# Kernel optimization log

Measured on AMD Instinct MI355X. Metric: run time of the kernel, lower is better.

Reference implementation:

```python
import jax, jax.numpy as jnp
import numpy as np

B = 512
IN_CORES = 12      # input_eff_capsules = 3072/256
N_PRIM = 12        # num_primary_capsules
N_PAR = 10         # num_parent_capsules
RFPC = 4           # receptive fields per capsule = 256/64
RF = 64            # receptive field size
CAP = 256          # capsule size
P_CONN = 0.2


def setup_inputs() -> dict:
    key = jax.random.key(0)
    ks = jax.random.split(key, 16)
    x = jax.random.uniform(ks[0], (B, 32, 32, 3), dtype=jnp.float32)
    # sparse 0/1 routing tensors (fixed Bernoulli(p) connectivity, stored as float params)
    C1 = jax.random.bernoulli(ks[1], P_CONN, (IN_CORES, RFPC, N_PRIM, RFPC)).astype(jnp.float32)
    C_skip = jax.random.bernoulli(ks[2], P_CONN, (IN_CORES, RFPC, N_PAR, RFPC)).astype(jnp.float32)
    C2 = jax.random.bernoulli(ks[3], P_CONN, (N_PRIM, RFPC, N_PAR, RFPC)).astype(jnp.float32)
    # per-receptive-field linear weights of the capsule layers
    s = 1.0 / np.sqrt(RF)
    W1 = jax.random.normal(ks[4], (N_PRIM, RFPC, RF, RF), dtype=jnp.float32) * s
    b1 = jnp.zeros((N_PRIM, RFPC, RF), dtype=jnp.float32)
    W2 = jax.random.normal(ks[5], (N_PAR, RFPC, RF, RF), dtype=jnp.float32) * s
    b2 = jnp.zeros((N_PAR, RFPC, RF), dtype=jnp.float32)
    # reconstruction MLP: 2560 -> 5000 -> 4000 -> 3072
    Wr1 = jax.random.normal(ks[6], (2560, 5000), dtype=jnp.float32) * (1.0 / np.sqrt(2560))
    br1 = jnp.zeros((5000,), dtype=jnp.float32)
    Wr2 = jax.random.normal(ks[7], (5000, 4000), dtype=jnp.float32) * (1.0 / np.sqrt(5000))
    br2 = jnp.zeros((4000,), dtype=jnp.float32)
    Wr3 = jax.random.normal(ks[8], (4000, 3072), dtype=jnp.float32) * (1.0 / np.sqrt(4000))
    br3 = jnp.zeros((3072,), dtype=jnp.float32)
    return {"x": x, "C1": C1, "W1": W1, "b1": b1, "C_skip": C_skip,
            "C2": C2, "W2": W2, "b2": b2,
            "Wr1": Wr1, "br1": br1, "Wr2": Wr2, "br2": br2, "Wr3": Wr3, "br3": br3}


def _caps_layer(x_flat, C, W, b):
    # x_flat: (B, in_cores*RFPC*RF); C: (in_cores, RFPC, out_caps, RFPC)
    bsz = x_flat.shape[0]
    in_cores = C.shape[0]
    xr = x_flat.reshape(bsz, in_cores, RFPC, RF)
    routed = jnp.einsum('ijkl,bijm->bklm', C, xr)          # (B, out_caps, RFPC, RF)
    out = jax.nn.relu(jnp.einsum('bklm,klmn->bkln', routed, W) + b)
    return out.reshape(bsz, -1)


def reference(x, C1, W1, b1, C_skip, C2, W2, b2, Wr1, br1, Wr2, br2, Wr3, br3):
    bsz = x.shape[0]
    # spatial_block_reshape: pure reshapes -> flatten
    x_flat = x.reshape(bsz, -1)                             # (B, 3072)
    # primary capsule layer
    x_prim = _caps_layer(x_flat, C1, W1, b1)                # (B, 3072)
    # skip connection: sparse routing einsum input->parent
    xr = x_prim.reshape(bsz, IN_CORES, RFPC, RF)
    x_skip = jnp.einsum('ijkl,bijm->bklm', C_skip, xr).reshape(bsz, -1)  # (B, 2560)
    # parent capsule layer + skip
    x_sum = x_skip + _caps_layer(x_prim, C2, W2, b2)        # (B, 2560)
    # top-1 capsule mask by norm
    norms = jnp.linalg.norm(x_sum.reshape(bsz, N_PAR, CAP), axis=-1)  # (B, 10)
    active = jnp.argmax(norms, axis=-1)                     # (B,)
    cap_id = jnp.arange(N_PAR * CAP) // CAP                 # (2560,)
    mask = (cap_id[None, :] == active[:, None]).astype(x_sum.dtype)
    x_recon = mask * x_sum
    # reconstruction MLP
    h = jax.nn.relu(x_recon @ Wr1 + br1)
    h = jax.nn.relu(h @ Wr2 + br2)
    out = jax.nn.sigmoid(h @ Wr3 + br3)                     # (B, 3072)
    return (out, x_sum)
```

## Files before the change

### kernel.cpp

```cpp
#include <hip/hip_runtime.h>
#include <math.h>


#define BATCH 512
#define OUT0_SZ (512*3072)

typedef __attribute__((ext_vector_type(8))) short short8;
typedef __attribute__((ext_vector_type(4))) float f32x4;

__device__ inline unsigned short f2bf(float f) {
    union { float f; unsigned u; } v; v.f = f;
    unsigned r = v.u + 0x7fffu + ((v.u >> 16) & 1u);
    return (unsigned short)(r >> 16);
}
__device__ inline float bf2f(unsigned int hi16) {
    union { unsigned u; float f; } v; v.u = hi16 << 16; return v.f;
}

#define GLD16(g, l) __builtin_amdgcn_global_load_lds( \
    (const __attribute__((address_space(1))) unsigned int*)(g), \
    (__attribute__((address_space(3))) unsigned int*)(l), 16, 0, 0)

struct CTJob {
    const float* W; unsigned short* Wt;
    int Kr, Nr, Kp, k0, n0;
};

__device__ inline CTJob ct_resolve(int bid,
    const float* Wr1, unsigned short* Wt1,
    const float* Wr2, unsigned short* Wt2,
    const float* Wr3, unsigned short* Wt3,
    const float* W1,  unsigned short* W1t,
    const float* W2,  unsigned short* W2t)
{
    CTJob j;
    int ktiles, rem;
    if (bid < 3200)       { j.W = Wr1; j.Wt = Wt1; j.Kr = 2560; j.Nr = 5000; j.Kp = 2560; ktiles = 40; rem = bid; }
    else if (bid < 8320)  { j.W = Wr2; j.Wt = Wt2; j.Kr = 5000; j.Nr = 4000; j.Kp = 5120; ktiles = 80; rem = bid - 3200; }
    else if (bid < 11392) { j.W = Wr3; j.Wt = Wt3; j.Kr = 4000; j.Nr = 3072; j.Kp = 4096; ktiles = 64; rem = bid - 8320; }
    else if (bid < 11440) { int kl = bid - 11392; j.W = W1 + (size_t)kl * 4096; j.Wt = W1t + (size_t)kl * 4096;
                            j.Kr = 64; j.Nr = 64; j.Kp = 64; ktiles = 1; rem = 0; }
    else                  { int kl = bid - 11440; j.W = W2 + (size_t)kl * 4096; j.Wt = W2t + (size_t)kl * 4096;
                            j.Kr = 64; j.Nr = 64; j.Kp = 64; ktiles = 1; rem = 0; }
    j.k0 = (rem % ktiles) * 64;
    j.n0 = (rem / ktiles) * 64;
    return j;
}

__device__ inline void ct_load(const CTJob& j, int tid, float4* v) {
    int kr = tid >> 4;
    int nc = (tid & 15) * 4;
    #pragma unroll
    for (int p = 0; p < 4; ++p) {
        int k = j.k0 + kr + p * 16;
        float4 vv = make_float4(0.f, 0.f, 0.f, 0.f);
        if (k < j.Kr) {
            if (j.n0 + nc + 3 < j.Nr) {
                vv = *(const float4*)&j.W[(size_t)k * j.Nr + j.n0 + nc];
            } else {
                float tmp[4] = {0.f, 0.f, 0.f, 0.f};
                #pragma unroll
                for (int jj = 0; jj < 4; ++jj)
                    if (j.n0 + nc + jj < j.Nr) tmp[jj] = j.W[(size_t)k * j.Nr + j.n0 + nc + jj];
                vv = make_float4(tmp[0], tmp[1], tmp[2], tmp[3]);
            }
        }
        v[p] = vv;
    }
}

__device__ inline void ct_stlds(float* t, int tid, const float4* v) {
    int kr = tid >> 4;
    int nc = (tid & 15) * 4;
    #pragma unroll
    for (int p = 0; p < 4; ++p) {
        float* row = &t[(kr + p * 16) * 65 + nc];
        row[0] = v[p].x; row[1] = v[p].y; row[2] = v[p].z; row[3] = v[p].w;
    }
}

__device__ inline void ct_pack(const CTJob& j, const float* t, int tid) {
    int nr = tid >> 2;
    int kc = (tid & 3) * 16;
    unsigned int u[8];
    #pragma unroll
    for (int jj = 0; jj < 8; ++jj) {
        float v0 = t[(kc + 2 * jj)     * 65 + nr];
        float v1 = t[(kc + 2 * jj + 1) * 65 + nr];
        u[jj] = (unsigned int)f2bf(v0) | ((unsigned int)f2bf(v1) << 16);
    }
    unsigned int* dst = (unsigned int*)&j.Wt[(size_t)(j.n0 + nr) * j.Kp + j.k0 + kc];
    *(uint4*)(dst)     = make_uint4(u[0], u[1], u[2], u[3]);
    *(uint4*)(dst + 4) = make_uint4(u[4], u[5], u[6], u[7]);
}

__global__ __launch_bounds__(256) void convT_all(
    const float* __restrict__ Wr1, unsigned short* __restrict__ Wt1,
    const float* __restrict__ Wr2, unsigned short* __restrict__ Wt2,
    const float* __restrict__ Wr3, unsigned short* __restrict__ Wt3,
    const float* __restrict__ W1,  unsigned short* __restrict__ W1t,
    const float* __restrict__ W2,  unsigned short* __restrict__ W2t)
{
    __shared__ float t[2][64 * 65];
    int tid = threadIdx.x;
    int tbase = blockIdx.x * 4;

    CTJob jc = ct_resolve(tbase, Wr1, Wt1, Wr2, Wt2, Wr3, Wt3, W1, W1t, W2, W2t);
    float4 v[4];
    ct_load(jc, tid, v);
    ct_stlds(t[0], tid, v);
    __syncthreads();

    #pragma unroll
    for (int i = 0; i < 4; ++i) {
        CTJob jn;
        float4 vn[4];
        if (i < 3) {
            jn = ct_resolve(tbase + i + 1, Wr1, Wt1, Wr2, Wt2, Wr3, Wt3, W1, W1t, W2, W2t);
            ct_load(jn, tid, vn);
        }
        ct_pack(jc, t[i & 1], tid);
        if (i < 3) {
            ct_stlds(t[(i + 1) & 1], tid, vn);
            jc = jn;
        }
        __syncthreads();
    }
}

__global__ __launch_bounds__(256) void caps_gemm1(
    const float* __restrict__ x, const float* __restrict__ C1,
    const unsigned short* __restrict__ W1t, const float* __restrict__ b1,
    unsigned short* __restrict__ xp)
{
    __shared__ __align__(16) unsigned short As[128 * 72];
    __shared__ __align__(16) unsigned short Bs[64 * 72];
    __shared__ float Csh[48];
    int kl = blockIdx.x;
    int bm = blockIdx.y * 128;
    int tid = threadIdx.x;
    int w = tid >> 6, lane = tid & 63, q = lane >> 4, r16 = lane & 15;
    int wm = (w >> 1) * 64, wn = (w & 1) * 32;

    if (tid < 48) Csh[tid] = C1[tid * 48 + kl];
    {
        const uint4* src = (const uint4*)(W1t + (size_t)kl * 4096);
        #pragma unroll
        for (int p = 0; p < 2; ++p) {
            int c = tid + p * 256;
            int row = c >> 3, cq = c & 7;
            *(uint4*)&Bs[row * 72 + cq * 8] = src[c];
        }
    }
    __syncthreads();

    int arow = tid >> 1, ah = (tid & 1) * 32;
    float accp[32];
    #pragma unroll
    for (int i = 0; i < 32; ++i) accp[i] = 0.f;
    const float* xrow = x + (size_t)(bm + arow) * 3072 + ah;
    for (int ij = 0; ij < 48; ++ij) {
        float c = Csh[ij];
        if (c != 0.f) {
            const float4* p4 = (const float4*)(xrow + ij * 64);
            #pragma unroll
            for (int cc = 0; cc < 8; ++cc) {
                float4 v = p4[cc];
                accp[cc * 4 + 0] = fmaf(c, v.x, accp[cc * 4 + 0]);
                accp[cc * 4 + 1] = fmaf(c, v.y, accp[cc * 4 + 1]);
                accp[cc * 4 + 2] = fmaf(c, v.z, accp[cc * 4 + 2]);
                accp[cc * 4 + 3] = fmaf(c, v.w, accp[cc * 4 + 3]);
            }
        }
    }
    {
        unsigned short* dst = &As[arow * 72 + ah];
        #pragma unroll
        for (int cc = 0; cc < 4; ++cc) {
            unsigned int u[4];
            #pragma unroll
            for (int j = 0; j < 4; ++j)
                u[j] = (unsigned int)f2bf(accp[cc * 8 + 2 * j]) |
                       ((unsigned int)f2bf(accp[cc * 8 + 2 * j + 1]) << 16);
            *(uint4*)&dst[cc * 8] = make_uint4(u[0], u[1], u[2], u[3]);
        }
    }
    __syncthreads();

    f32x4 acc[4][2];
    #pragma unroll
    for (int i = 0; i < 4; ++i)
        #pragma unroll
        for (int j = 0; j < 2; ++j) acc[i][j] = (f32x4)0.f;
    #pragma unroll
    for (int ks = 0; ks < 2; ++ks) {
        short8 a[4], b[2];
        #pragma unroll
        for (int mt = 0; mt < 4; ++mt)
            a[mt] = *(const short8*)&As[(wm + mt * 16 + r16) * 72 + ks * 32 + q * 8];
        #pragma unroll
        for (int nt = 0; nt < 2; ++nt)
            b[nt] = *(const short8*)&Bs[(wn + nt * 16 + r16) * 72 + ks * 32 + q * 8];
        #pragma unroll
        for (int mt = 0; mt < 4; ++mt)
            #pragma unroll
            for (int nt = 0; nt < 2; ++nt)
                acc[mt][nt] = __builtin_amdgcn_mfma_f32_16x16x32_bf16(a[mt], b[nt], acc[mt][nt], 0, 0, 0);
    }

    #pragma unroll
    for (int mt = 0; mt < 4; ++mt) {
        #pragma unroll
        for (int nt = 0; nt < 2; ++nt) {
            int n = wn + nt * 16 + r16;
            float bv = b1[kl * 64 + n];
            #pragma unroll
            for (int reg = 0; reg < 4; ++reg) {
                int row = bm + wm + mt * 16 + q * 4 + reg;
                xp[(size_t)row * 3072 + kl * 64 + n] = f2bf(fmaxf(acc[mt][nt][reg] + bv, 0.f));
            }
        }
    }
}

__global__ __launch_bounds__(256) void caps_gemm2(
    const unsigned short* __restrict__ xp, const float* __restrict__ Cs,
    const float* __restrict__ C2, const unsigned short* __restrict__ W2t,
    const float* __restrict__ b2, float* __restrict__ xsum,
    float* __restrict__ part8)
{
    __shared__ __align__(16) unsigned short As[128 * 72];
    __shared__ __align__(16) unsigned short Bs[64 * 72];
    __shared__ __align__(16) float Sk[128 * 68];
    __shared__ float C2sh[48], Cssh[48];
    int kl = blockIdx.x;
    int bm = blockIdx.y * 128;
    int tid = threadIdx.x;
    int w = tid >> 6, lane = tid & 63, q = lane >> 4, r16 = lane & 15;
    int wm = (w >> 1) * 64, wn = (w & 1) * 32;
    int half = w & 1;

    if (tid < 48) { C2sh[tid] = C2[tid * 40 + kl]; Cssh[tid] = Cs[tid * 40 + kl]; }
    {
        const uint4* src = (const uint4*)(W2t + (size_t)kl * 4096);
        #pragma unroll
        for (int p = 0; p < 2; ++p) {
            int c = tid + p * 256;
            int row = c >> 3, cq = c & 7;
            *(uint4*)&Bs[row * 72 + cq * 8] = src[c];
        }
    }
    __syncthreads();

    int arow = tid >> 1, ah = (tid & 1) * 32;
    float accp[32], skp[32];
    #pragma unroll
    for (int i = 0; i < 32; ++i) { accp[i] = 0.f; skp[i] = 0.f; }
    const unsigned short* xprow = xp + (size_t)(bm + arow) * 3072 + ah;
    for (int ij = 0; ij < 48; ++ij) {
        float c2 = C2sh[ij], cs = Cssh[ij];
        if (c2 != 0.f || cs != 0.f) {
            const uint4* p4 = (const uint4*)(xprow + ij * 64);
            #pragma unroll
            for (int cc = 0; cc < 4; ++cc) {
                uint4 v = p4[cc];
                unsigned int uu[4] = {v.x, v.y, v.z, v.w};
                #pragma unroll
                for (int j = 0; j < 4; ++j) {
                    float lo = bf2f(uu[j] & 0xffffu);
                    float hi = bf2f(uu[j] >> 16);
                    int idx = cc * 8 + 2 * j;
                    accp[idx]     = fmaf(c2, lo, accp[idx]);
                    accp[idx + 1] = fmaf(c2, hi, accp[idx + 1]);
                    skp[idx]      = fmaf(cs, lo, skp[idx]);
                    skp[idx + 1]  = fmaf(cs, hi, skp[idx + 1]);
                }
            }
        }
    }
    {
        unsigned short* dst = &As[arow * 72 + ah];
        #pragma unroll
        for (int cc = 0; cc < 4; ++cc) {
            unsigned int u[4];
            #pragma unroll
            for (int j = 0; j < 4; ++j)
                u[j] = (unsigned int)f2bf(accp[cc * 8 + 2 * j]) |
                       ((unsigned int)f2bf(accp[cc * 8 + 2 * j + 1]) << 16);
            *(uint4*)&dst[cc * 8] = make_uint4(u[0], u[1], u[2], u[3]);
        }
        float* sdst = &Sk[arow * 68 + ah];
        #pragma unroll
        for (int cc = 0; cc < 8; ++cc)
            *(float4*)&sdst[cc * 4] = make_float4(skp[cc*4], skp[cc*4+1], skp[cc*4+2], skp[cc*4+3]);
    }
    __syncthreads();

    f32x4 acc[4][2];
    #pragma unroll
    for (int i = 0; i < 4; ++i)
        #pragma unroll
        for (int j = 0; j < 2; ++j) acc[i][j] = (f32x4)0.f;
    #pragma unroll
    for (int ks = 0; ks < 2; ++ks) {
        short8 a[4], b[2];
        #pragma unroll
        for (int mt = 0; mt < 4; ++mt)
            a[mt] = *(const short8*)&As[(wm + mt * 16 + r16) * 72 + ks * 32 + q * 8];
        #pragma unroll
        for (int nt = 0; nt < 2; ++nt)
            b[nt] = *(const short8*)&Bs[(wn + nt * 16 + r16) * 72 + ks * 32 + q * 8];
        #pragma unroll
        for (int mt = 0; mt < 4; ++mt)
            #pragma unroll
            for (int nt = 0; nt < 2; ++nt)
                acc[mt][nt] = __builtin_amdgcn_mfma_f32_16x16x32_bf16(a[mt], b[nt], acc[mt][nt], 0, 0, 0);
    }

    #pragma unroll
    for (int mt = 0; mt < 4; ++mt) {
        float sreg[4] = {0.f, 0.f, 0.f, 0.f};
        #pragma unroll
        for (int nt = 0; nt < 2; ++nt) {
            int n = wn + nt * 16 + r16;
            float bv = b2[kl * 64 + n];
            #pragma unroll
            for (int reg = 0; reg < 4; ++reg) {
                int lr = wm + mt * 16 + q * 4 + reg;
                float v = Sk[lr * 68 + n] + fmaxf(acc[mt][nt][reg] + bv, 0.f);
                xsum[(size_t)(bm + lr) * 2560 + kl * 64 + n] = v;
                sreg[reg] += v * v;
            }
        }
        #pragma unroll
        for (int reg = 0; reg < 4; ++reg) {
            float s = sreg[reg];
            s += __shfl_xor(s, 1); s += __shfl_xor(s, 2);
            s += __shfl_xor(s, 4); s += __shfl_xor(s, 8);
            if (r16 == 0) {
                int row = bm + wm + mt * 16 + q * 4 + reg;
                part8[(size_t)row * 80 + kl * 2 + half] = s;
            }
        }
    }
}

__global__ __launch_bounds__(256) void mask_kernel(
    const float* __restrict__ xs, const float* __restrict__ part8,
    unsigned short* __restrict__ xrec, int* __restrict__ active)
{
    int b = blockIdx.x;
    int tid = threadIdx.x;
    __shared__ float norms[10];
    __shared__ int act_sh;
    if (tid < 10) {
        float s = 0.f;
        #pragma unroll
        for (int j = 0; j < 8; ++j) s += part8[(size_t)b * 80 + tid * 8 + j];
        norms[tid] = s;
    }
    __syncthreads();
    if (tid == 0) {
        int best = 0; float bn = -1.f;
        #pragma unroll
        for (int k = 0; k < 10; ++k)
            if (norms[k] > bn) { bn = norms[k]; best = k; }
        act_sh = best;
        active[b] = best;
    }
    __syncthreads();
    int act = act_sh;
    int idx = act * 256 + tid;
    xrec[(size_t)b * 2560 + idx] = f2bf(xs[(size_t)b * 2560 + idx]);
}

__global__ __launch_bounds__(512) void bucket_kernel(
    const int* __restrict__ active, int* __restrict__ perm,
    int4* __restrict__ slots)
{
    __shared__ int cnt[10], pos[10];
    int tid = threadIdx.x;
    if (tid < 10) cnt[tid] = 0;
    __syncthreads();
    int a = active[tid];
    atomicAdd(&cnt[a], 1);
    __syncthreads();
    if (tid == 0) {
        int o = 0, s = 0;
        for (int g = 0; g < 10; ++g) {
            pos[g] = o;
            int mg = cnt[g];
            for (int t0 = 0; t0 < mg; t0 += 64)
                slots[s++] = make_int4(g, o + t0, min(64, mg - t0), 0);
            o += mg;
        }
        for (; s < 18; ++s) slots[s] = make_int4(0, 0, 0, 0);
    }
    __syncthreads();
    int r = atomicAdd(&pos[a], 1);
    perm[r] = tid;
}

__global__ __launch_bounds__(256) void gemm_l1(
    const unsigned short* __restrict__ xrec, const int* __restrict__ perm,
    const int4* __restrict__ slots, const unsigned short* __restrict__ Wt1,
    const float* __restrict__ br1, unsigned short* __restrict__ h1)
{
    int4 s = slots[blockIdx.y];
    if (s.z == 0) return;
    int g = s.x, mstart = s.y, mval = s.z;
    int bn = blockIdx.x * 128;
    int tid = threadIdx.x;

    __shared__ __align__(16) unsigned short As[64 * 32];
    __shared__ __align__(16) unsigned short Bs[128 * 32];
    __shared__ int rows[64];
    if (tid < 64) rows[tid] = perm[mstart + min(tid, mval - 1)];
    __syncthreads();

    int w = tid >> 6, lane = tid & 63;
    int wm = (w >> 1) * 32, wn = (w & 1) * 64;
    int q = lane >> 4, r16 = lane & 15;
    int srow = tid >> 2, skq = tid & 3;

    f32x4 acc[2][4];
    #pragma unroll
    for (int i = 0; i < 2; ++i)
        #pragma unroll
        for (int j = 0; j < 4; ++j) acc[i][j] = (f32x4)0.f;

    int arow = rows[srow];
    const unsigned short* ga = xrec + (size_t)arow * 2560 + g * 256 + skq * 8;
    const unsigned short* gb = Wt1 + (size_t)(bn + srow) * 2560 + g * 256 + skq * 8;

    for (int kk = 0; kk < 256; kk += 32) {
        GLD16(ga + kk, &As[tid * 8]);
        GLD16(gb + kk, &Bs[tid * 8]);
        GLD16(gb + kk + (size_t)64 * 2560, &Bs[(tid + 256) * 8]);
        __syncthreads();

        short8 a[2], b[4];
        #pragma unroll
        for (int mt = 0; mt < 2; ++mt)
            a[mt] = *(const short8*)&As[(wm + mt * 16 + r16) * 32 + q * 8];
        #pragma unroll
        for (int nt = 0; nt < 4; ++nt)
            b[nt] = *(const short8*)&Bs[(wn + nt * 16 + r16) * 32 + q * 8];
        #pragma unroll
        for (int mt = 0; mt < 2; ++mt)
            #pragma unroll
            for (int nt = 0; nt < 4; ++nt)
                acc[mt][nt] = __builtin_amdgcn_mfma_f32_16x16x32_bf16(a[mt], b[nt], acc[mt][nt], 0, 0, 0);
        __syncthreads();
    }

    #pragma unroll
    for (int mt = 0; mt < 2; ++mt) {
        #pragma unroll
        for (int nt = 0; nt < 4; ++nt) {
            int n = bn + wn + nt * 16 + r16;
            float bv = (n < 5000) ? br1[n] : 0.f;
            #pragma unroll
            for (int reg = 0; reg < 4; ++reg) {
                int lm = wm + mt * 16 + q * 4 + reg;
                if (lm < mval)
                    h1[(size_t)(mstart + lm) * 5120 + n] =
                        f2bf(fmaxf(acc[mt][nt][reg] + bv, 0.f));
            }
        }
    }
}

#define SPLITK 4
__global__ __launch_bounds__(256) void gemm_splitk(
    const unsigned short* __restrict__ A, int ldA,
    const unsigned short* __restrict__ Bt, int ldB,
    float* __restrict__ P, int Np, int kper)
{
    __shared__ __align__(16) unsigned short As[64 * 32];
    __shared__ __align__(16) unsigned short Bs[128 * 32];

    int tid = threadIdx.x;
    int bn = blockIdx.x * 128;
    int bm = blockIdx.y * 64;
    int kz = blockIdx.z * kper;

    int w = tid >> 6, lane = tid & 63;
    int wm = (w >> 1) * 32, wn = (w & 1) * 64;
    int q = lane >> 4, r16 = lane & 15;

    int srow = tid >> 2, skq = tid & 3;

    f32x4 acc[2][4];
    #pragma unroll
    for (int i = 0; i < 2; ++i)
        #pragma unroll
        for (int j = 0; j < 4; ++j) acc[i][j] = (f32x4)0.f;

    for (int kk = 0; kk < kper; kk += 32) {
        int k0 = kz + kk;
        const unsigned short* ga = A + (size_t)(bm + srow) * ldA + k0 + skq * 8;
        GLD16(ga, &As[tid * 8]);
        const unsigned short* gb = Bt + (size_t)(bn + srow) * ldB + k0 + skq * 8;
        GLD16(gb, &Bs[tid * 8]);
        GLD16(gb + (size_t)64 * ldB, &Bs[(tid + 256) * 8]);
        __syncthreads();

        short8 a[2], b[4];
        #pragma unroll
        for (int mt = 0; mt < 2; ++mt)
            a[mt] = *(const short8*)&As[(wm + mt * 16 + r16) * 32 + q * 8];
        #pragma unroll
        for (int nt = 0; nt < 4; ++nt)
            b[nt] = *(const short8*)&Bs[(wn + nt * 16 + r16) * 32 + q * 8];
        #pragma unroll
        for (int mt = 0; mt < 2; ++mt)
            #pragma unroll
            for (int nt = 0; nt < 4; ++nt)
                acc[mt][nt] = __builtin_amdgcn_mfma_f32_16x16x32_bf16(a[mt], b[nt], acc[mt][nt], 0, 0, 0);
        __syncthreads();
    }

    float* Pz = P + (size_t)blockIdx.z * 512 * Np;
    #pragma unroll
    for (int mt = 0; mt < 2; ++mt) {
        #pragma unroll
        for (int nt = 0; nt < 4; ++nt) {
            int cn = bn + wn + nt * 16 + r16;
            #pragma unroll
            for (int reg = 0; reg < 4; ++reg) {
                int cm = bm + wm + mt * 16 + q * 4 + reg;
                Pz[(size_t)cm * Np + cn] = acc[mt][nt][reg];
            }
        }
    }
}

template<int MODE>
__global__ __launch_bounds__(256) void combine_kernel(
    const float* __restrict__ P, const float* __restrict__ bias,
    void* __restrict__ out, int Np, int N_real, const int* __restrict__ perm)
{
    int gid = blockIdx.x * 256 + threadIdx.x;
    int n0 = (gid * 4) % Np;
    int m  = (gid * 4) / Np;
    size_t MN = (size_t)512 * Np;
    const float* p = P + (size_t)m * Np + n0;
    f32x4 s = *(const f32x4*)p;
    s += *(const f32x4*)(p + MN);
    s += *(const f32x4*)(p + 2 * MN);
    s += *(const f32x4*)(p + 3 * MN);
    f32x4 bv = (n0 < N_real) ? *(const f32x4*)(bias + n0) : (f32x4)0.f;
    s += bv;
    if (MODE == 0) {
        unsigned int lo = (unsigned int)f2bf(fmaxf(s[0], 0.f)) | ((unsigned int)f2bf(fmaxf(s[1], 0.f)) << 16);
        unsigned int hi = (unsigned int)f2bf(fmaxf(s[2], 0.f)) | ((unsigned int)f2bf(fmaxf(s[3], 0.f)) << 16);
        *(uint2*)((unsigned short*)out + (size_t)m * Np + n0) = make_uint2(lo, hi);
    } else {
        int row = perm[m];
        f32x4 v;
        v[0] = 1.f / (1.f + expf(-s[0]));
        v[1] = 1.f / (1.f + expf(-s[1]));
        v[2] = 1.f / (1.f + expf(-s[2]));
        v[3] = 1.f / (1.f + expf(-s[3]));
        *(f32x4*)((float*)out + (size_t)row * Np + n0) = v;
    }
}

extern "C" void kernel_launch(void* const* d_in, const int* in_sizes, int n_in,
                              void* d_out, int out_size, void* d_ws, size_t ws_size,
                              hipStream_t stream) {
    const float* x   = (const float*)d_in[0];
    const float* C1  = (const float*)d_in[1];
    const float* W1  = (const float*)d_in[2];
    const float* b1  = (const float*)d_in[3];
    const float* Cs  = (const float*)d_in[4];
    const float* C2  = (const float*)d_in[5];
    const float* W2  = (const float*)d_in[6];
    const float* b2  = (const float*)d_in[7];
    const float* Wr1 = (const float*)d_in[8];
    const float* br1 = (const float*)d_in[9];
    const float* Wr2 = (const float*)d_in[10];
    const float* br2 = (const float*)d_in[11];
    const float* Wr3 = (const float*)d_in[12];
    const float* br3 = (const float*)d_in[13];

    float* out = (float*)d_out;
    float* out0     = out;
    float* xsum_out = out + OUT0_SZ;

    char* base = (char*)d_ws;
    unsigned short* xrec  = (unsigned short*)(base);
    unsigned short* h1    = (unsigned short*)(base +   2621440);
    unsigned short* h2    = (unsigned short*)(base +   7864320);
    unsigned short* Wt1   = (unsigned short*)(base +  12058624);
    unsigned short* Wt2   = (unsigned short*)(base +  38273024);
    unsigned short* Wt3   = (unsigned short*)(base +  80216064);
    float*          Pbuf  = (float*)(base + 105381888);
    unsigned short* xp    = (unsigned short*)(base + 147324928);
    unsigned short* W1t   = (unsigned short*)(base + 150470656);
    unsigned short* W2t   = (unsigned short*)(base + 150863872);
    float*          part8 = (float*)(base + 151191552);
    int*  active = (int*)(base + 105381888 + 33554432);
    int*  perm   = active + 512;
    int4* slots  = (int4*)(perm + 512);

    convT_all<<<2870, 256, 0, stream>>>(Wr1, Wt1, Wr2, Wt2, Wr3, Wt3,
                                        W1, W1t, W2, W2t);

    caps_gemm1<<<dim3(48, 4), 256, 0, stream>>>(x, C1, W1t, b1, xp);
    caps_gemm2<<<dim3(40, 4), 256, 0, stream>>>(xp, Cs, C2, W2t, b2, xsum_out, part8);
    mask_kernel<<<BATCH, 256, 0, stream>>>(xsum_out, part8, xrec, active);
    bucket_kernel<<<1, 512, 0, stream>>>(active, perm, slots);

    gemm_l1<<<dim3(5120 / 128, 18), 256, 0, stream>>>(xrec, perm, slots, Wt1, br1, h1);

    gemm_splitk<<<dim3(4096 / 128, 8, SPLITK), 256, 0, stream>>>(h1, 5120, Wt2, 5120, Pbuf, 4096, 5120 / SPLITK);
    combine_kernel<0><<<512 * 4096 / 1024, 256, 0, stream>>>(Pbuf, br2, h2, 4096, 4000, nullptr);

    gemm_splitk<<<dim3(3072 / 128, 8, SPLITK), 256, 0, stream>>>(h2, 4096, Wt3, 4096, Pbuf, 3072, 4096 / SPLITK);
    combine_kernel<1><<<512 * 3072 / 1024, 256, 0, stream>>>(Pbuf, br3, out0, 3072, 3072, perm);
}
```

Baseline: 384.5 us.

## Read fp32 MLP weights directly in GEMMs and drop the transpose-convert pass

Removes the separate kernel that converted and transposed all three reconstruction weight matrices to bf16 on every call. The GEMMs now load the fp32 weights straight from global memory into registers, convert them to bf16, and store them into swizzled, double-buffered LDS tiles, so global loads overlap the MFMA work. Activation buffers get padded leading dimensions, and caps_gemm2 writes its skip partials into xsum directly instead of staging them in LDS. This saves one full write and re-read of the weights, but the GEMMs now read fp32, twice the bytes per weight tile, and redo the conversion for every M tile.

```diff
diff --git a/kernel.cpp b/kernel.cpp
--- a/kernel.cpp
+++ b/kernel.cpp
@@ -4,6 +4,13 @@
 
 #define BATCH 512
 #define OUT0_SZ (512*3072)
+
+#define LD_XREC 2576
+#define LD_H1 5136
+#define LD_H2 4112
+#define LDP2 4224
+#define LDP3 3200
+#define SPLITK 4
 
 typedef __attribute__((ext_vector_type(8))) short short8;
 typedef __attribute__((ext_vector_type(4))) float f32x4;
@@ -21,111 +28,89 @@
     (const __attribute__((address_space(1))) unsigned int*)(g), \
     (__attribute__((address_space(3))) unsigned int*)(l), 16, 0, 0)
 
-struct CTJob {
+struct BReg { float4 r0, r1, r2, r3; };
+
+__device__ inline void loadB(BReg& br, const float* B, int ldB, int Kr, int Nr,
+                             int k0, int bn, int tid)
+{
+    int kq = tid >> 5, f4c = tid & 31;
+    int ka = k0 + kq * 4;
+    int nb = bn + f4c * 4;
+    float4 z = make_float4(0.f, 0.f, 0.f, 0.f);
+    br.r0 = z; br.r1 = z; br.r2 = z; br.r3 = z;
+    const float* p = B + (size_t)ka * ldB + nb;
+    if (nb + 3 < Nr) {
+        if (ka + 3 < Kr) {
+            br.r0 = *(const float4*)p;
+            br.r1 = *(const float4*)(p + ldB);
+            br.r2 = *(const float4*)(p + 2 * (size_t)ldB);
+            br.r3 = *(const float4*)(p + 3 * (size_t)ldB);
+        } else {
+            if (ka     < Kr) br.r0 = *(const float4*)p;
+            if (ka + 1 < Kr) br.r1 = *(const float4*)(p + ldB);
+            if (ka + 2 < Kr) br.r2 = *(const float4*)(p + 2 * (size_t)ldB);
+            if (ka + 3 < Kr) br.r3 = *(const float4*)(p + 3 * (size_t)ldB);
+        }
+    } else {
+        float t[4][4] = {};
+        #pragma unroll
+        for (int e = 0; e < 4; ++e)
+            if (ka + e < Kr)
+                #pragma unroll
+                for (int j = 0; j < 4; ++j)
+                    if (nb + j < Nr) t[e][j] = B[(size_t)(ka + e) * ldB + nb + j];
+        br.r0 = make_float4(t[0][0], t[0][1], t[0][2], t[0][3]);
+        br.r1 = make_float4(t[1][0], t[1][1], t[1][2], t[1][3]);
+        br.r2 = make_float4(t[2][0], t[2][1], t[2][2], t[2][3]);
+        br.r3 = make_float4(t[3][0], t[3][1], t[3][2], t[3][3]);
+    }
+}
+
+__device__ inline void writeB(const BReg& br, unsigned short* Bs, int tid)
+{
+    int kq = tid >> 5, f4c = tid & 31;
+    int kqs = kq ^ ((f4c & 3) << 1);
+    uint2* B2 = (uint2*)Bs;
+    float a0[4] = {br.r0.x, br.r0.y, br.r0.z, br.r0.w};
+    float a1[4] = {br.r1.x, br.r1.y, br.r1.z, br.r1.w};
+    float a2[4] = {br.r2.x, br.r2.y, br.r2.z, br.r2.w};
+    float a3[4] = {br.r3.x, br.r3.y, br.r3.z, br.r3.w};
+    #pragma unroll
+    for (int j = 0; j < 4; ++j) {
+        unsigned int u0 = (unsigned)f2bf(a0[j]) | ((unsigned)f2bf(a1[j]) << 16);
+        unsigned int u1 = (unsigned)f2bf(a2[j]) | ((unsigned)f2bf(a3[j]) << 16);
+        B2[(f4c * 4 + j) * 10 + kqs] = make_uint2(u0, u1);
+    }
+}
+
+__device__ inline short8 readB(const unsigned short* Bs, int n, int q)
+{
+    int sw = ((n >> 2) & 3) << 1;
+    return *(const short8*)&Bs[n * 40 + ((2 * q) ^ sw) * 4];
+}
+
+__global__ __launch_bounds__(256) void conv_small(
+    const float* __restrict__ W1, unsigned short* __restrict__ W1t,
+    const float* __restrict__ W2, unsigned short* __restrict__ W2t)
+{
+    int bid = blockIdx.x;
     const float* W; unsigned short* Wt;
-    int Kr, Nr, Kp, k0, n0;
-};
-
-__device__ inline CTJob ct_resolve(int bid,
-    const float* Wr1, unsigned short* Wt1,
-    const float* Wr2, unsigned short* Wt2,
-    const float* Wr3, unsigned short* Wt3,
-    const float* W1,  unsigned short* W1t,
-    const float* W2,  unsigned short* W2t)
-{
-    CTJob j;
-    int ktiles, rem;
-    if (bid < 3200)       { j.W = Wr1; j.Wt = Wt1; j.Kr = 2560; j.Nr = 5000; j.Kp = 2560; ktiles = 40; rem = bid; }
-    else if (bid < 8320)  { j.W = Wr2; j.Wt = Wt2; j.Kr = 5000; j.Nr = 4000; j.Kp = 5120; ktiles = 80; rem = bid - 3200; }
-    else if (bid < 11392) { j.W = Wr3; j.Wt = Wt3; j.Kr = 4000; j.Nr = 3072; j.Kp = 4096; ktiles = 64; rem = bid - 8320; }
-    else if (bid < 11440) { int kl = bid - 11392; j.W = W1 + (size_t)kl * 4096; j.Wt = W1t + (size_t)kl * 4096;
-                            j.Kr = 64; j.Nr = 64; j.Kp = 64; ktiles = 1; rem = 0; }
-    else                  { int kl = bid - 11440; j.W = W2 + (size_t)kl * 4096; j.Wt = W2t + (size_t)kl * 4096;
-                            j.Kr = 64; j.Nr = 64; j.Kp = 64; ktiles = 1; rem = 0; }
-    j.k0 = (rem % ktiles) * 64;
-    j.n0 = (rem / ktiles) * 64;
-    return j;
-}
-
-__device__ inline void ct_load(const CTJob& j, int tid, float4* v) {
-    int kr = tid >> 4;
-    int nc = (tid & 15) * 4;
-    #pragma unroll
-    for (int p = 0; p < 4; ++p) {
-        int k = j.k0 + kr + p * 16;
-        float4 vv = make_float4(0.f, 0.f, 0.f, 0.f);
-        if (k < j.Kr) {
-            if (j.n0 + nc + 3 < j.Nr) {
-                vv = *(const float4*)&j.W[(size_t)k * j.Nr + j.n0 + nc];
-            } else {
-                float tmp[4] = {0.f, 0.f, 0.f, 0.f};
-                #pragma unroll
-                for (int jj = 0; jj < 4; ++jj)
-                    if (j.n0 + nc + jj < j.Nr) tmp[jj] = j.W[(size_t)k * j.Nr + j.n0 + nc + jj];
-                vv = make_float4(tmp[0], tmp[1], tmp[2], tmp[3]);
-            }
-        }
-        v[p] = vv;
-    }
-}
-
-__device__ inline void ct_stlds(float* t, int tid, const float4* v) {
-    int kr = tid >> 4;
-    int nc = (tid & 15) * 4;
-    #pragma unroll
-    for (int p = 0; p < 4; ++p) {
-        float* row = &t[(kr + p * 16) * 65 + nc];
-        row[0] = v[p].x; row[1] = v[p].y; row[2] = v[p].z; row[3] = v[p].w;
-    }
-}
-
-__device__ inline void ct_pack(const CTJob& j, const float* t, int tid) {
+    if (bid < 48) { W = W1 + (size_t)bid * 4096; Wt = W1t + (size_t)bid * 4096; }
+    else          { W = W2 + (size_t)(bid - 48) * 4096; Wt = W2t + (size_t)(bid - 48) * 4096; }
+    int tid = threadIdx.x;
     int nr = tid >> 2;
     int kc = (tid & 3) * 16;
+    float v[16];
+    #pragma unroll
+    for (int i = 0; i < 16; ++i)
+        v[i] = W[(size_t)(kc + i) * 64 + nr];
     unsigned int u[8];
     #pragma unroll
-    for (int jj = 0; jj < 8; ++jj) {
-        float v0 = t[(kc + 2 * jj)     * 65 + nr];
-        float v1 = t[(kc + 2 * jj + 1) * 65 + nr];
-        u[jj] = (unsigned int)f2bf(v0) | ((unsigned int)f2bf(v1) << 16);
-    }
-    unsigned int* dst = (unsigned int*)&j.Wt[(size_t)(j.n0 + nr) * j.Kp + j.k0 + kc];
+    for (int j = 0; j < 8; ++j)
+        u[j] = (unsigned int)f2bf(v[2 * j]) | ((unsigned int)f2bf(v[2 * j + 1]) << 16);
+    unsigned int* dst = (unsigned int*)&Wt[(size_t)nr * 64 + kc];
     *(uint4*)(dst)     = make_uint4(u[0], u[1], u[2], u[3]);
     *(uint4*)(dst + 4) = make_uint4(u[4], u[5], u[6], u[7]);
-}
-
-__global__ __launch_bounds__(256) void convT_all(
-    const float* __restrict__ Wr1, unsigned short* __restrict__ Wt1,
-    const float* __restrict__ Wr2, unsigned short* __restrict__ Wt2,
-    const float* __restrict__ Wr3, unsigned short* __restrict__ Wt3,
-    const float* __restrict__ W1,  unsigned short* __restrict__ W1t,
-    const float* __restrict__ W2,  unsigned short* __restrict__ W2t)
-{
-    __shared__ float t[2][64 * 65];
-    int tid = threadIdx.x;
-    int tbase = blockIdx.x * 4;
-
-    CTJob jc = ct_resolve(tbase, Wr1, Wt1, Wr2, Wt2, Wr3, Wt3, W1, W1t, W2, W2t);
-    float4 v[4];
-    ct_load(jc, tid, v);
-    ct_stlds(t[0], tid, v);
-    __syncthreads();
-
-    #pragma unroll
-    for (int i = 0; i < 4; ++i) {
-        CTJob jn;
-        float4 vn[4];
-        if (i < 3) {
-            jn = ct_resolve(tbase + i + 1, Wr1, Wt1, Wr2, Wt2, Wr3, Wt3, W1, W1t, W2, W2t);
-            ct_load(jn, tid, vn);
-        }
-        ct_pack(jc, t[i & 1], tid);
-        if (i < 3) {
-            ct_stlds(t[(i + 1) & 1], tid, vn);
-            jc = jn;
-        }
-        __syncthreads();
-    }
 }
 
 __global__ __launch_bounds__(256) void caps_gemm1(
@@ -231,7 +216,6 @@
 {
     __shared__ __align__(16) unsigned short As[128 * 72];
     __shared__ __align__(16) unsigned short Bs[64 * 72];
-    __shared__ __align__(16) float Sk[128 * 68];
     __shared__ float C2sh[48], Cssh[48];
     int kl = blockIdx.x;
     int bm = blockIdx.y * 128;
@@ -289,10 +273,10 @@
                        ((unsigned int)f2bf(accp[cc * 8 + 2 * j + 1]) << 16);
             *(uint4*)&dst[cc * 8] = make_uint4(u[0], u[1], u[2], u[3]);
         }
-        float* sdst = &Sk[arow * 68 + ah];
+        float* sx = xsum + (size_t)(bm + arow) * 2560 + kl * 64 + ah;
         #pragma unroll
         for (int cc = 0; cc < 8; ++cc)
-            *(float4*)&sdst[cc * 4] = make_float4(skp[cc*4], skp[cc*4+1], skp[cc*4+2], skp[cc*4+3]);
+            *(float4*)&sx[cc * 4] = make_float4(skp[cc*4], skp[cc*4+1], skp[cc*4+2], skp[cc*4+3]);
     }
     __syncthreads();
 
@@ -327,8 +311,9 @@
             #pragma unroll
             for (int reg = 0; reg < 4; ++reg) {
                 int lr = wm + mt * 16 + q * 4 + reg;
-                float v = Sk[lr * 68 + n] + fmaxf(acc[mt][nt][reg] + bv, 0.f);
-                xsum[(size_t)(bm + lr) * 2560 + kl * 64 + n] = v;
+                size_t xi = (size_t)(bm + lr) * 2560 + kl * 64 + n;
+                float v = xsum[xi] + fmaxf(acc[mt][nt][reg] + bv, 0.f);
+                xsum[xi] = v;
                 sreg[reg] += v * v;
             }
         }
@@ -371,7 +356,7 @@
     __syncthreads();
     int act = act_sh;
     int idx = act * 256 + tid;
-    xrec[(size_t)b * 2560 + idx] = f2bf(xs[(size_t)b * 2560 + idx]);
+    xrec[(size_t)b * LD_XREC + idx] = f2bf(xs[(size_t)b * 2560 + idx]);
 }
 
 __global__ __launch_bounds__(512) void bucket_kernel(
@@ -403,18 +388,19 @@
 
 __global__ __launch_bounds__(256) void gemm_l1(
     const unsigned short* __restrict__ xrec, const int* __restrict__ perm,
-    const int4* __restrict__ slots, const unsigned short* __restrict__ Wt1,
+    const int4* __restrict__ slots, const float* __restrict__ Wr1,
     const float* __restrict__ br1, unsigned short* __restrict__ h1)
 {
+    __shared__ __align__(16) unsigned short As[2][64 * 32];
+    __shared__ __align__(16) unsigned short Bs[2][128 * 40];
+    __shared__ int rows[64];
+
     int4 s = slots[blockIdx.y];
     if (s.z == 0) return;
     int g = s.x, mstart = s.y, mval = s.z;
     int bn = blockIdx.x * 128;
     int tid = threadIdx.x;
 
-    __shared__ __align__(16) unsigned short As[64 * 32];
-    __shared__ __align__(16) unsigned short Bs[128 * 32];
-    __shared__ int rows[64];
     if (tid < 64) rows[tid] = perm[mstart + min(tid, mval - 1)];
     __syncthreads();
 
@@ -430,28 +416,37 @@
         for (int j = 0; j < 4; ++j) acc[i][j] = (f32x4)0.f;
 
     int arow = rows[srow];
-    const unsigned short* ga = xrec + (size_t)arow * 2560 + g * 256 + skq * 8;
-    const unsigned short* gb = Wt1 + (size_t)(bn + srow) * 2560 + g * 256 + skq * 8;
-
-    for (int kk = 0; kk < 256; kk += 32) {
-        GLD16(ga + kk, &As[tid * 8]);
-        GLD16(gb + kk, &Bs[tid * 8]);
-        GLD16(gb + kk + (size_t)64 * 2560, &Bs[(tid + 256) * 8]);
-        __syncthreads();
-
+    const unsigned short* ga = xrec + (size_t)arow * LD_XREC + g * 256 + skq * 8;
+    int kbase = g * 256;
+
+    BReg br;
+    loadB(br, Wr1, 5000, 2560, 5000, kbase, bn, tid);
+    GLD16(ga, &As[0][tid * 8]);
+    writeB(br, Bs[0], tid);
+    __syncthreads();
+
+    int cur = 0;
+    for (int kk = 32; kk <= 256; kk += 32) {
+        bool more = kk < 256;
+        if (more) {
+            GLD16(ga + kk, &As[cur ^ 1][tid * 8]);
+            loadB(br, Wr1, 5000, 2560, 5000, kbase + kk, bn, tid);
+        }
         short8 a[2], b[4];
         #pragma unroll
         for (int mt = 0; mt < 2; ++mt)
-            a[mt] = *(const short8*)&As[(wm + mt * 16 + r16) * 32 + q * 8];
+            a[mt] = *(const short8*)&As[cur][(wm + mt * 16 + r16) * 32 + q * 8];
         #pragma unroll
         for (int nt = 0; nt < 4; ++nt)
-            b[nt] = *(const short8*)&Bs[(wn + nt * 16 + r16) * 32 + q * 8];
+            b[nt] = readB(Bs[cur], wn + nt * 16 + r16, q);
         #pragma unroll
         for (int mt = 0; mt < 2; ++mt)
             #pragma unroll
             for (int nt = 0; nt < 4; ++nt)
                 acc[mt][nt] = __builtin_amdgcn_mfma_f32_16x16x32_bf16(a[mt], b[nt], acc[mt][nt], 0, 0, 0);
+        if (more) writeB(br, Bs[cur ^ 1], tid);
         __syncthreads();
+        cur ^= 1;
     }
 
     #pragma unroll
@@ -464,21 +459,20 @@
             for (int reg = 0; reg < 4; ++reg) {
                 int lm = wm + mt * 16 + q * 4 + reg;
                 if (lm < mval)
-                    h1[(size_t)(mstart + lm) * 5120 + n] =
+                    h1[(size_t)(mstart + lm) * LD_H1 + n] =
                         f2bf(fmaxf(acc[mt][nt][reg] + bv, 0.f));
             }
         }
     }
 }
 
-#define SPLITK 4
 __global__ __launch_bounds__(256) void gemm_splitk(
     const unsigned short* __restrict__ A, int ldA,
-    const unsigned short* __restrict__ Bt, int ldB,
-    float* __restrict__ P, int Np, int kper)
-{
-    __shared__ __align__(16) unsigned short As[64 * 32];
-    __shared__ __align__(16) unsigned short Bs[128 * 32];
+    const float* __restrict__ B, int ldB, int Kr, int Nr,
+    float* __restrict__ P, int ldP, int kper)
+{
+    __shared__ __align__(16) unsigned short As[2][64 * 32];
+    __shared__ __align__(16) unsigned short Bs[2][128 * 40];
 
     int tid = threadIdx.x;
     int bn = blockIdx.x * 128;
@@ -488,7 +482,6 @@
     int w = tid >> 6, lane = tid & 63;
     int wm = (w >> 1) * 32, wn = (w & 1) * 64;
     int q = lane >> 4, r16 = lane & 15;
-
     int srow = tid >> 2, skq = tid & 3;
 
     f32x4 acc[2][4];
@@ -497,31 +490,39 @@
         #pragma unroll
         for (int j = 0; j < 4; ++j) acc[i][j] = (f32x4)0.f;
 
-    for (int kk = 0; kk < kper; kk += 32) {
-        int k0 = kz + kk;
-        const unsigned short* ga = A + (size_t)(bm + srow) * ldA + k0 + skq * 8;
-        GLD16(ga, &As[tid * 8]);
-        const unsigned short* gb = Bt + (size_t)(bn + srow) * ldB + k0 + skq * 8;
-        GLD16(gb, &Bs[tid * 8]);
-        GLD16(gb + (size_t)64 * ldB, &Bs[(tid + 256) * 8]);
-        __syncthreads();
-
+    const unsigned short* ga = A + (size_t)(bm + srow) * ldA + kz + skq * 8;
+
+    BReg br;
+    loadB(br, B, ldB, Kr, Nr, kz, bn, tid);
+    GLD16(ga, &As[0][tid * 8]);
+    writeB(br, Bs[0], tid);
+    __syncthreads();
+
+    int cur = 0;
+    for (int kk = 32; kk <= kper; kk += 32) {
+        bool more = kk < kper;
+        if (more) {
+            GLD16(ga + kk, &As[cur ^ 1][tid * 8]);
+            loadB(br, B, ldB, Kr, Nr, kz + kk, bn, tid);
+        }
         short8 a[2], b[4];
         #pragma unroll
         for (int mt = 0; mt < 2; ++mt)
-            a[mt] = *(const short8*)&As[(wm + mt * 16 + r16) * 32 + q * 8];
+            a[mt] = *(const short8*)&As[cur][(wm + mt * 16 + r16) * 32 + q * 8];
         #pragma unroll
         for (int nt = 0; nt < 4; ++nt)
-            b[nt] = *(const short8*)&Bs[(wn + nt * 16 + r16) * 32 + q * 8];
+            b[nt] = readB(Bs[cur], wn + nt * 16 + r16, q);
         #pragma unroll
         for (int mt = 0; mt < 2; ++mt)
             #pragma unroll
             for (int nt = 0; nt < 4; ++nt)
                 acc[mt][nt] = __builtin_amdgcn_mfma_f32_16x16x32_bf16(a[mt], b[nt], acc[mt][nt], 0, 0, 0);
+        if (more) writeB(br, Bs[cur ^ 1], tid);
         __syncthreads();
-    }
-
-    float* Pz = P + (size_t)blockIdx.z * 512 * Np;
+        cur ^= 1;
+    }
+
+    float* Pz = P + (size_t)blockIdx.z * 512 * ldP;
     #pragma unroll
     for (int mt = 0; mt < 2; ++mt) {
         #pragma unroll
@@ -530,7 +531,7 @@
             #pragma unroll
             for (int reg = 0; reg < 4; ++reg) {
                 int cm = bm + wm + mt * 16 + q * 4 + reg;
-                Pz[(size_t)cm * Np + cn] = acc[mt][nt][reg];
+                Pz[(size_t)cm * ldP + cn] = acc[mt][nt][reg];
             }
         }
     }
@@ -538,14 +539,15 @@
 
 template<int MODE>
 __global__ __launch_bounds__(256) void combine_kernel(
-    const float* __restrict__ P, const float* __restrict__ bias,
-    void* __restrict__ out, int Np, int N_real, const int* __restrict__ perm)
+    const float* __restrict__ P, int ldP, const float* __restrict__ bias,
+    void* __restrict__ out, int ldO, int Np, int N_real,
+    const int* __restrict__ perm)
 {
     int gid = blockIdx.x * 256 + threadIdx.x;
     int n0 = (gid * 4) % Np;
     int m  = (gid * 4) / Np;
-    size_t MN = (size_t)512 * Np;
-    const float* p = P + (size_t)m * Np + n0;
+    size_t MN = (size_t)512 * ldP;
+    const float* p = P + (size_t)m * ldP + n0;
     f32x4 s = *(const f32x4*)p;
     s += *(const f32x4*)(p + MN);
     s += *(const f32x4*)(p + 2 * MN);
@@ -555,7 +557,7 @@
     if (MODE == 0) {
         unsigned int lo = (unsigned int)f2bf(fmaxf(s[0], 0.f)) | ((unsigned int)f2bf(fmaxf(s[1], 0.f)) << 16);
         unsigned int hi = (unsigned int)f2bf(fmaxf(s[2], 0.f)) | ((unsigned int)f2bf(fmaxf(s[3], 0.f)) << 16);
-        *(uint2*)((unsigned short*)out + (size_t)m * Np + n0) = make_uint2(lo, hi);
+        *(uint2*)((unsigned short*)out + (size_t)m * ldO + n0) = make_uint2(lo, hi);
     } else {
         int row = perm[m];
         f32x4 v;
@@ -563,7 +565,7 @@
         v[1] = 1.f / (1.f + expf(-s[1]));
         v[2] = 1.f / (1.f + expf(-s[2]));
         v[3] = 1.f / (1.f + expf(-s[3]));
-        *(f32x4*)((float*)out + (size_t)row * Np + n0) = v;
+        *(f32x4*)((float*)out + (size_t)row * ldO + n0) = v;
     }
 }
 
@@ -590,34 +592,34 @@
     float* xsum_out = out + OUT0_SZ;
 
     char* base = (char*)d_ws;
-    unsigned short* xrec  = (unsigned short*)(base);
-    unsigned short* h1    = (unsigned short*)(base +   2621440);
-    unsigned short* h2    = (unsigned short*)(base +   7864320);
-    unsigned short* Wt1   = (unsigned short*)(base +  12058624);
-    unsigned short* Wt2   = (unsigned short*)(base +  38273024);
-    unsigned short* Wt3   = (unsigned short*)(base +  80216064);
-    float*          Pbuf  = (float*)(base + 105381888);
-    unsigned short* xp    = (unsigned short*)(base + 147324928);
-    unsigned short* W1t   = (unsigned short*)(base + 150470656);
-    unsigned short* W2t   = (unsigned short*)(base + 150863872);
-    float*          part8 = (float*)(base + 151191552);
-    int*  active = (int*)(base + 105381888 + 33554432);
+    unsigned short* xrec = (unsigned short*)(base);
+    unsigned short* h1   = (unsigned short*)(base +  2637824);
+    unsigned short* h2   = (unsigned short*)(base +  7897088);
+    unsigned short* xp   = (unsigned short*)(base + 12107776);
+    unsigned short* W1t  = (unsigned short*)(base + 15253504);
+    unsigned short* W2t  = (unsigned short*)(base + 15646720);
+    float*          part8= (float*)(base + 15974400);
+    int*  active = (int*)(base + 16138240);
     int*  perm   = active + 512;
     int4* slots  = (int4*)(perm + 512);
-
-    convT_all<<<2870, 256, 0, stream>>>(Wr1, Wt1, Wr2, Wt2, Wr3, Wt3,
-                                        W1, W1t, W2, W2t);
+    float*          Pbuf = (float*)(base + 16144384);
+
+    conv_small<<<88, 256, 0, stream>>>(W1, W1t, W2, W2t);
 
     caps_gemm1<<<dim3(48, 4), 256, 0, stream>>>(x, C1, W1t, b1, xp);
     caps_gemm2<<<dim3(40, 4), 256, 0, stream>>>(xp, Cs, C2, W2t, b2, xsum_out, part8);
     mask_kernel<<<BATCH, 256, 0, stream>>>(xsum_out, part8, xrec, active);
     bucket_kernel<<<1, 512, 0, stream>>>(active, perm, slots);
 
-    gemm_l1<<<dim3(5120 / 128, 18), 256, 0, stream>>>(xrec, perm, slots, Wt1, br1, h1);
-
-    gemm_splitk<<<dim3(4096 / 128, 8, SPLITK), 256, 0, stream>>>(h1, 5120, Wt2, 5120, Pbuf, 4096, 5120 / SPLITK);
-    combine_kernel<0><<<512 * 4096 / 1024, 256, 0, stream>>>(Pbuf, br2, h2, 4096, 4000, nullptr);
-
-    gemm_splitk<<<dim3(3072 / 128, 8, SPLITK), 256, 0, stream>>>(h2, 4096, Wt3, 4096, Pbuf, 3072, 4096 / SPLITK);
-    combine_kernel<1><<<512 * 3072 / 1024, 256, 0, stream>>>(Pbuf, br3, out0, 3072, 3072, perm);
-}
+    gemm_l1<<<dim3(5120 / 128, 18), 256, 0, stream>>>(xrec, perm, slots, Wr1, br1, h1);
+
+    gemm_splitk<<<dim3(4096 / 128, 8, SPLITK), 256, 0, stream>>>(
+        h1, LD_H1, Wr2, 4000, 5000, 4000, Pbuf, LDP2, 5120 / SPLITK);
+    combine_kernel<0><<<512 * 4096 / 1024, 256, 0, stream>>>(
+        Pbuf, LDP2, br2, h2, LD_H2, 4096, 4000, nullptr);
+
+    gemm_splitk<<<dim3(3072 / 128, 8, SPLITK), 256, 0, stream>>>(
+        h2, LD_H2, Wr3, 3072, 4000, 3072, Pbuf, LDP3, 4096 / SPLITK);
+    combine_kernel<1><<<512 * 3072 / 1024, 256, 0, stream>>>(
+        Pbuf, LDP3, br3, out0, 3072, 3072, 3072, perm);
+}
```

Result: no change. 385.7 us (+0.3%).
